# Performance work log

Hardware: AMD Instinct MI355X
Metric: run time of the kernel (lower is better)

## Reference

```python
import jax, jax.numpy as jnp
import numpy as np

N, M, D = 256, 1024, 512


def setup_inputs() -> dict:
    key = jax.random.key(0)
    ks = jax.random.split(key, 12)
    s = 1.0 / np.sqrt(D)
    return {
        "q": jax.random.normal(ks[0], (N, D), jnp.float32),
        "k": jax.random.normal(ks[1], (M, D), jnp.float32),
        "v": jax.random.normal(ks[2], (M, D), jnp.float32),
        "mask": jax.random.randint(ks[3], (N, M), 0, 2, jnp.int32),
        "WQ": jax.random.normal(ks[4], (D, D), jnp.float32) * s,
        "bQ": jax.random.normal(ks[5], (D,), jnp.float32) * s,
        "WK": jax.random.normal(ks[6], (D, D), jnp.float32) * s,
        "bK": jax.random.normal(ks[7], (D,), jnp.float32) * s,
        "WV": jax.random.normal(ks[8], (D, D), jnp.float32) * s,
        "bV": jax.random.normal(ks[9], (D,), jnp.float32) * s,
        "Ww": jax.random.normal(ks[10], (1, D), jnp.float32) * s,
        "bw": jax.random.normal(ks[11], (1,), jnp.float32) * s,
    }


def reference(q, k, v, mask, WQ, bQ, WK, bK, WV, bV, Ww, bw):
    # Linear projections (torch Linear: x @ W.T + b)
    qp = q @ WQ.T + bQ            # [N, D]
    kp = k @ WK.T + bK            # [M, D]
    vp = v @ WV.T + bV            # [M, D]
    # Additive (Bahdanau) scores: tanh(q_n + k_m) . w  -> [N, M]
    t = jnp.tanh(qp[:, None, :] + kp[None, :, :])   # [N, M, D]
    score = jnp.einsum("nmd,d->nm", t, Ww[0]) + bw[0]
    score = jnp.where(mask == 1, score, jnp.float32(-1e6))
    w = jax.nn.softmax(score, axis=1)               # softmax over keys (dim 1)
    context = jnp.einsum("nm,md->nd", w, vp)        # weighted sum over keys
    return context
```

## Files before the change

kernel.cpp:

```cpp
#include <hip/hip_runtime.h>

#define NQ 256
#define MK 1024
#define DD 512
#define CSC 2.8853900817779268f
#define L2E 1.4426950408889634f

typedef __attribute__((ext_vector_type(8))) short short8;
typedef __attribute__((ext_vector_type(4))) float floatx4;

__device__ inline int swz(int i, int d)
{
    return (((i >> 4) * 16 + (d >> 5)) << 9) | (((d >> 3) & 3) << 7)
         | ((i & 15) << 3) | (d & 7);
}

__device__ inline void bsplit(float x, unsigned short& h, unsigned short& l)
{
    unsigned u = __float_as_uint(x);
    unsigned hr = (u + 0x7FFFu + ((u >> 16) & 1u)) >> 16;
    h = (unsigned short)hr;
    float hf = __uint_as_float(hr << 16);
    unsigned ul = __float_as_uint(x - hf);
    l = (unsigned short)((ul + 0x7FFFu + ((ul >> 16) & 1u)) >> 16);
}

__global__ __launch_bounds__(256) void convert_split(
    const float* __restrict__ q, const float* __restrict__ k, const float* __restrict__ v,
    const float* __restrict__ WQ, const float* __restrict__ WK, const float* __restrict__ WV,
    unsigned short* __restrict__ qhi, unsigned short* __restrict__ qlo,
    unsigned short* __restrict__ khi, unsigned short* __restrict__ klo,
    unsigned short* __restrict__ vhi, unsigned short* __restrict__ vlo,
    unsigned short* __restrict__ wqhi, unsigned short* __restrict__ wqlo,
    unsigned short* __restrict__ wkhi, unsigned short* __restrict__ wklo,
    unsigned short* __restrict__ wvhi, unsigned short* __restrict__ wvlo)
{
    const int i4 = blockIdx.x * 256 + threadIdx.x;
    const float* src; unsigned short *dh, *dl; int li;
    if (i4 < 32768)       { src = q;  dh = qhi;  dl = qlo;  li = i4; }
    else if (i4 < 163840) { src = k;  dh = khi;  dl = klo;  li = i4 - 32768; }
    else if (i4 < 294912) { src = v;  dh = vhi;  dl = vlo;  li = i4 - 163840; }
    else if (i4 < 360448) { src = WQ; dh = wqhi; dl = wqlo; li = i4 - 294912; }
    else if (i4 < 425984) { src = WK; dh = wkhi; dl = wklo; li = i4 - 360448; }
    else                  { src = WV; dh = wvhi; dl = wvlo; li = i4 - 425984; }

    float4 x = *(const float4*)&src[li * 4];
    ushort4 h, l;
    bsplit(x.x, h.x, l.x); bsplit(x.y, h.y, l.y);
    bsplit(x.z, h.z, l.z); bsplit(x.w, h.w, l.w);

    const int e = li * 4;
    const int o = swz(e >> 9, e & 511);
    *(ushort4*)&dh[o] = h;
    *(ushort4*)&dl[o] = l;
}

__global__ __launch_bounds__(256) void proj_mfma(
    const unsigned short* __restrict__ qhi, const unsigned short* __restrict__ qlo,
    const unsigned short* __restrict__ khi, const unsigned short* __restrict__ klo,
    const unsigned short* __restrict__ vhi, const unsigned short* __restrict__ vlo,
    const unsigned short* __restrict__ wqhi, const unsigned short* __restrict__ wqlo,
    const unsigned short* __restrict__ wkhi, const unsigned short* __restrict__ wklo,
    const unsigned short* __restrict__ wvhi, const unsigned short* __restrict__ wvlo,
    const float* __restrict__ bQ, const float* __restrict__ bK, const float* __restrict__ bV,
    float* __restrict__ qs, float* __restrict__ kts, float* __restrict__ vp)
{
    int t = blockIdx.x;
    const unsigned short *Xh, *Xl, *Wh, *Wl; const float* b; int mode;
    if (t < 32)       { mode = 0; Xh = qhi; Xl = qlo; Wh = wqhi; Wl = wqlo; b = bQ; }
    else if (t < 160) { mode = 1; t -= 32;  Xh = khi; Xl = klo; Wh = wkhi; Wl = wklo; b = bK; }
    else              { mode = 2; t -= 160; Xh = vhi; Xl = vlo; Wh = wvhi; Wl = wvlo; b = bV; }
    const int i0 = (t >> 3) * 64;
    const int j0 = (t & 7) * 64;

    const int l  = threadIdx.x & 63;
    const int w  = threadIdx.x >> 6;
    const int lr = l & 15;
    const int rbase = (l >> 4) * 4;

    const unsigned short* Ah = Xh + ((i0 >> 4) + w) * 8192 + l * 8;
    const unsigned short* Al = Xl + ((i0 >> 4) + w) * 8192 + l * 8;
    const unsigned short* Bh = Wh + (j0 >> 4) * 8192 + l * 8;
    const unsigned short* Bl = Wl + (j0 >> 4) * 8192 + l * 8;

    floatx4 acc[4] = {{0,0,0,0},{0,0,0,0},{0,0,0,0},{0,0,0,0}};

#pragma unroll
    for (int kc = 0; kc < 16; ++kc) {
        short8 ah = *(const short8*)(Ah + kc * 512);
        short8 al = *(const short8*)(Al + kc * 512);
#pragma unroll
        for (int nt = 0; nt < 4; ++nt) {
            short8 bh = *(const short8*)(Bh + nt * 8192 + kc * 512);
            short8 bl = *(const short8*)(Bl + nt * 8192 + kc * 512);
            acc[nt] = __builtin_amdgcn_mfma_f32_16x16x32_bf16(ah, bh, acc[nt], 0, 0, 0);
            acc[nt] = __builtin_amdgcn_mfma_f32_16x16x32_bf16(ah, bl, acc[nt], 0, 0, 0);
            acc[nt] = __builtin_amdgcn_mfma_f32_16x16x32_bf16(al, bh, acc[nt], 0, 0, 0);
        }
    }

    if (mode == 1) {
#pragma unroll
        for (int nt = 0; nt < 4; ++nt) {
            const int d = j0 + nt * 16 + lr;
            const float bb = b[d];
            float* base = &kts[(((d >> 3) * MK) + i0 + w * 16 + rbase) * 8 + (d & 7)];
#pragma unroll
            for (int j = 0; j < 4; ++j)
                base[j * 8] = (acc[nt][j] + bb) * CSC;
        }
    } else {
        float* dst = (mode == 0) ? qs : vp;
        const float sc = (mode == 0) ? CSC : 1.0f;
#pragma unroll
        for (int nt = 0; nt < 4; ++nt) {
            const float bb = b[j0 + nt * 16 + lr];
#pragma unroll
            for (int j = 0; j < 4; ++j)
                dst[(i0 + w * 16 + rbase + j) * DD + j0 + nt * 16 + lr]
                    = (acc[nt][j] + bb) * sc;
        }
    }
}

__global__ __launch_bounds__(1024) void score_sm(
    const float* __restrict__ qs, const float* __restrict__ kts,
    const float* __restrict__ Ww, const int* __restrict__ mask,
    float* __restrict__ S)
{
    const int n = blockIdx.x;
    const int t = threadIdx.x;
    const int lane = t & 63, wave = t >> 6;

    __shared__ float qw[DD * 2];
    __shared__ float red[16];

    if (t < DD) { qw[t * 2] = qs[n * DD + t]; qw[t * 2 + 1] = Ww[t]; }
    __syncthreads();

    const float* kp = kts + t * 8;
    float acc = 0.f;
    for (int c = 0; c < 64; ++c) {
        float4 k0 = *(const float4*)(kp + c * (MK * 8));
        float4 k1 = *(const float4*)(kp + c * (MK * 8) + 4);
        float kv[8] = {k0.x, k0.y, k0.z, k0.w, k1.x, k1.y, k1.z, k1.w};
#pragma unroll
        for (int j = 0; j < 8; ++j) {
            float2 wq = *(const float2*)&qw[(c * 8 + j) * 2];
            float e = __builtin_amdgcn_exp2f(wq.x + kv[j]);
            acc = fmaf(wq.y, __builtin_amdgcn_rcpf(e + 1.0f), acc);
        }
    }

    float s = -2.0f * acc;
    s = (mask[n * MK + t] == 1) ? s : -1e6f;

    float mx = s;
    for (int o = 32; o > 0; o >>= 1) mx = fmaxf(mx, __shfl_xor(mx, o, 64));
    if (lane == 0) red[wave] = mx;
    __syncthreads();
    if (wave == 0) {
        float r = red[lane & 15];
        for (int o = 8; o > 0; o >>= 1) r = fmaxf(r, __shfl_xor(r, o, 64));
        if (lane == 0) red[0] = r;
    }
    __syncthreads();
    mx = red[0];
    __syncthreads();

    float e = __builtin_amdgcn_exp2f((s - mx) * L2E);
    float sum = e;
    for (int o = 32; o > 0; o >>= 1) sum += __shfl_xor(sum, o, 64);
    if (lane == 0) red[wave] = sum;
    __syncthreads();
    if (wave == 0) {
        float r = red[lane & 15];
        for (int o = 8; o > 0; o >>= 1) r += __shfl_xor(r, o, 64);
        if (lane == 0) red[0] = r;
    }
    __syncthreads();
    sum = red[0];

    S[n * MK + t] = e * __builtin_amdgcn_rcpf(sum);
}

#define CNG 8
#define CMC 256

__global__ __launch_bounds__(512) void context_v2(const float* __restrict__ S,
                                                  const float* __restrict__ vp,
                                                  float* __restrict__ out)
{
    __shared__ float ws[CMC][12];
    const int t = threadIdx.x;
    const int n0 = blockIdx.x * CNG;
    const int m0 = blockIdx.y * CMC;

#pragma unroll
    for (int p = 0; p < 4; ++p) {
        int e = t + p * 512;
        int m = e & 255, n = e >> 8;
        ws[m][n] = S[(n0 + n) * MK + m0 + m];
    }
    __syncthreads();

    float acc[CNG] = {};
    for (int m = 0; m < CMC; ++m) {
        float vv = vp[(m0 + m) * DD + t];
        float4 w0 = *(const float4*)&ws[m][0];
        float4 w4 = *(const float4*)&ws[m][4];
        acc[0] = fmaf(w0.x, vv, acc[0]);
        acc[1] = fmaf(w0.y, vv, acc[1]);
        acc[2] = fmaf(w0.z, vv, acc[2]);
        acc[3] = fmaf(w0.w, vv, acc[3]);
        acc[4] = fmaf(w4.x, vv, acc[4]);
        acc[5] = fmaf(w4.y, vv, acc[5]);
        acc[6] = fmaf(w4.z, vv, acc[6]);
        acc[7] = fmaf(w4.w, vv, acc[7]);
    }
#pragma unroll
    for (int n = 0; n < CNG; ++n) atomicAdd(&out[(n0 + n) * DD + t], acc[n]);
}

extern "C" void kernel_launch(void* const* d_in, const int* in_sizes, int n_in,
                              void* d_out, int out_size, void* d_ws, size_t ws_size,
                              hipStream_t stream)
{
    const float* q    = (const float*)d_in[0];
    const float* k    = (const float*)d_in[1];
    const float* v    = (const float*)d_in[2];
    const int*   mask = (const int*)  d_in[3];
    const float* WQ   = (const float*)d_in[4];
    const float* bQ   = (const float*)d_in[5];
    const float* WK   = (const float*)d_in[6];
    const float* bK   = (const float*)d_in[7];
    const float* WV   = (const float*)d_in[8];
    const float* bV   = (const float*)d_in[9];
    const float* Ww   = (const float*)d_in[10];
    const float* bw   = (const float*)d_in[11];
    (void)bw;
    float* out = (float*)d_out;

    float* qs  = (float*)d_ws;
    float* kts = qs + NQ * DD;
    float* vp  = kts + DD * MK;
    float* S   = vp + MK * DD;
    unsigned short* p16  = (unsigned short*)(S + NQ * MK);
    unsigned short* qhi  = p16;              p16 += NQ * DD;
    unsigned short* qlo  = p16;              p16 += NQ * DD;
    unsigned short* khi  = p16;              p16 += MK * DD;
    unsigned short* klo  = p16;              p16 += MK * DD;
    unsigned short* vhi  = p16;              p16 += MK * DD;
    unsigned short* vlo  = p16;              p16 += MK * DD;
    unsigned short* wqhi = p16;              p16 += DD * DD;
    unsigned short* wqlo = p16;              p16 += DD * DD;
    unsigned short* wkhi = p16;              p16 += DD * DD;
    unsigned short* wklo = p16;              p16 += DD * DD;
    unsigned short* wvhi = p16;              p16 += DD * DD;
    unsigned short* wvlo = p16;

    hipMemsetAsync(d_out, 0, (size_t)NQ * DD * sizeof(float), stream);

    convert_split<<<1920, 256, 0, stream>>>(q, k, v, WQ, WK, WV,
        qhi, qlo, khi, klo, vhi, vlo, wqhi, wqlo, wkhi, wklo, wvhi, wvlo);

    proj_mfma<<<288, 256, 0, stream>>>(qhi, qlo, khi, klo, vhi, vlo,
        wqhi, wqlo, wkhi, wklo, wvhi, wvlo, bQ, bK, bV, qs, kts, vp);

    score_sm<<<NQ, 1024, 0, stream>>>(qs, kts, Ww, mask, S);

    context_v2<<<dim3(NQ / CNG, MK / CMC), dim3(512), 0, stream>>>(S, vp, out);
}
```

Measured before the change: 158.4 us.

## Precompute exponentials of projections to remove exp from score loop; drop context atomics

Projection epilogue now stores exp2 of the scaled q and k projections, so the score inner loop computes tanh via a product instead of an exp per element. The k loads in the score loop are software-prefetched one chunk ahead. The context kernel is restructured to reduce over all keys within a block via shared memory, removing the atomics and the output memset. Factoring exp(a+b) into a product risks overflow/precision loss for large projection magnitudes.

After: 144.7 us. -8.7%, faster.

```diff
diff --git a/kernel.cpp b/kernel.cpp
--- a/kernel.cpp
+++ b/kernel.cpp
@@ -63,7 +63,7 @@
     const unsigned short* __restrict__ wkhi, const unsigned short* __restrict__ wklo,
     const unsigned short* __restrict__ wvhi, const unsigned short* __restrict__ wvlo,
     const float* __restrict__ bQ, const float* __restrict__ bK, const float* __restrict__ bV,
-    float* __restrict__ qs, float* __restrict__ kts, float* __restrict__ vp)
+    float* __restrict__ qe, float* __restrict__ ke, float* __restrict__ vp)
 {
     int t = blockIdx.x;
     const unsigned short *Xh, *Xl, *Wh, *Wl; const float* b; int mode;
@@ -104,27 +104,28 @@
         for (int nt = 0; nt < 4; ++nt) {
             const int d = j0 + nt * 16 + lr;
             const float bb = b[d];
-            float* base = &kts[(((d >> 3) * MK) + i0 + w * 16 + rbase) * 8 + (d & 7)];
+            float* base = &ke[(((d >> 3) * MK) + i0 + w * 16 + rbase) * 8 + (d & 7)];
 #pragma unroll
             for (int j = 0; j < 4; ++j)
-                base[j * 8] = (acc[nt][j] + bb) * CSC;
+                base[j * 8] = __builtin_amdgcn_exp2f((acc[nt][j] + bb) * CSC);
         }
     } else {
-        float* dst = (mode == 0) ? qs : vp;
-        const float sc = (mode == 0) ? CSC : 1.0f;
+        float* dst = (mode == 0) ? qe : vp;
 #pragma unroll
         for (int nt = 0; nt < 4; ++nt) {
             const float bb = b[j0 + nt * 16 + lr];
 #pragma unroll
-            for (int j = 0; j < 4; ++j)
-                dst[(i0 + w * 16 + rbase + j) * DD + j0 + nt * 16 + lr]
-                    = (acc[nt][j] + bb) * sc;
+            for (int j = 0; j < 4; ++j) {
+                float val = acc[nt][j] + bb;
+                if (mode == 0) val = __builtin_amdgcn_exp2f(val * CSC);
+                dst[(i0 + w * 16 + rbase + j) * DD + j0 + nt * 16 + lr] = val;
+            }
         }
     }
 }
 
 __global__ __launch_bounds__(1024) void score_sm(
-    const float* __restrict__ qs, const float* __restrict__ kts,
+    const float* __restrict__ qe, const float* __restrict__ kts,
     const float* __restrict__ Ww, const int* __restrict__ mask,
     float* __restrict__ S)
 {
@@ -135,21 +136,29 @@
     __shared__ float qw[DD * 2];
     __shared__ float red[16];
 
-    if (t < DD) { qw[t * 2] = qs[n * DD + t]; qw[t * 2 + 1] = Ww[t]; }
+    if (t < DD) { qw[t * 2] = qe[n * DD + t]; qw[t * 2 + 1] = Ww[t]; }
     __syncthreads();
 
     const float* kp = kts + t * 8;
     float acc = 0.f;
+    float4 k0 = *(const float4*)(kp);
+    float4 k1 = *(const float4*)(kp + 4);
     for (int c = 0; c < 64; ++c) {
-        float4 k0 = *(const float4*)(kp + c * (MK * 8));
-        float4 k1 = *(const float4*)(kp + c * (MK * 8) + 4);
+        float4 p0 = k0, p1 = k1;
+        if (c + 1 < 64) {
+            p0 = *(const float4*)(kp + (c + 1) * (MK * 8));
+            p1 = *(const float4*)(kp + (c + 1) * (MK * 8) + 4);
+        }
         float kv[8] = {k0.x, k0.y, k0.z, k0.w, k1.x, k1.y, k1.z, k1.w};
 #pragma unroll
-        for (int j = 0; j < 8; ++j) {
-            float2 wq = *(const float2*)&qw[(c * 8 + j) * 2];
-            float e = __builtin_amdgcn_exp2f(wq.x + kv[j]);
-            acc = fmaf(wq.y, __builtin_amdgcn_rcpf(e + 1.0f), acc);
-        }
+        for (int j = 0; j < 8; j += 2) {
+            float4 qq = *(const float4*)&qw[(c * 8 + j) * 2];
+            float e0 = qq.x * kv[j];
+            float e1 = qq.z * kv[j + 1];
+            acc = fmaf(qq.y, __builtin_amdgcn_rcpf(e0 + 1.0f), acc);
+            acc = fmaf(qq.w, __builtin_amdgcn_rcpf(e1 + 1.0f), acc);
+        }
+        k0 = p0; k1 = p1;
     }
 
     float s = -2.0f * acc;
@@ -184,42 +193,47 @@
     S[n * MK + t] = e * __builtin_amdgcn_rcpf(sum);
 }
 
-#define CNG 8
-#define CMC 256
-
-__global__ __launch_bounds__(512) void context_v2(const float* __restrict__ S,
+#define XNG 4
+
+__global__ __launch_bounds__(512) void context_v3(const float* __restrict__ S,
                                                   const float* __restrict__ vp,
                                                   float* __restrict__ out)
 {
-    __shared__ float ws[CMC][12];
+    __shared__ float ws[MK][XNG];
+    __shared__ float pacc[4][XNG][128];
     const int t = threadIdx.x;
-    const int n0 = blockIdx.x * CNG;
-    const int m0 = blockIdx.y * CMC;
-
-#pragma unroll
-    for (int p = 0; p < 4; ++p) {
+    const int n0 = blockIdx.x * XNG;
+    const int d0 = blockIdx.y * 128;
+
+#pragma unroll
+    for (int p = 0; p < 8; ++p) {
         int e = t + p * 512;
-        int m = e & 255, n = e >> 8;
-        ws[m][n] = S[(n0 + n) * MK + m0 + m];
-    }
-    __syncthreads();
-
-    float acc[CNG] = {};
-    for (int m = 0; m < CMC; ++m) {
-        float vv = vp[(m0 + m) * DD + t];
-        float4 w0 = *(const float4*)&ws[m][0];
-        float4 w4 = *(const float4*)&ws[m][4];
-        acc[0] = fmaf(w0.x, vv, acc[0]);
-        acc[1] = fmaf(w0.y, vv, acc[1]);
-        acc[2] = fmaf(w0.z, vv, acc[2]);
-        acc[3] = fmaf(w0.w, vv, acc[3]);
-        acc[4] = fmaf(w4.x, vv, acc[4]);
-        acc[5] = fmaf(w4.y, vv, acc[5]);
-        acc[6] = fmaf(w4.z, vv, acc[6]);
-        acc[7] = fmaf(w4.w, vv, acc[7]);
-    }
-#pragma unroll
-    for (int n = 0; n < CNG; ++n) atomicAdd(&out[(n0 + n) * DD + t], acc[n]);
+        int nn = e >> 10, m = e & 1023;
+        ws[m][nn] = S[(n0 + nn) * MK + m];
+    }
+    __syncthreads();
+
+    const int d = d0 + (t & 127);
+    const int seg = t >> 7;
+    float acc[XNG] = {};
+    for (int m = seg * 256; m < seg * 256 + 256; ++m) {
+        float vv = vp[m * DD + d];
+        float4 w = *(const float4*)&ws[m][0];
+        acc[0] = fmaf(w.x, vv, acc[0]);
+        acc[1] = fmaf(w.y, vv, acc[1]);
+        acc[2] = fmaf(w.z, vv, acc[2]);
+        acc[3] = fmaf(w.w, vv, acc[3]);
+    }
+#pragma unroll
+    for (int nn = 0; nn < XNG; ++nn) pacc[seg][nn][t & 127] = acc[nn];
+    __syncthreads();
+
+    if (t < XNG * 128) {
+        int nn = t >> 7, dd = t & 127;
+        float r = pacc[0][nn][dd] + pacc[1][nn][dd]
+                + pacc[2][nn][dd] + pacc[3][nn][dd];
+        out[(n0 + nn) * DD + d0 + dd] = r;
+    }
 }
 
 extern "C" void kernel_launch(void* const* d_in, const int* in_sizes, int n_in,
@@ -241,9 +255,9 @@
     (void)bw;
     float* out = (float*)d_out;
 
-    float* qs  = (float*)d_ws;
-    float* kts = qs + NQ * DD;
-    float* vp  = kts + DD * MK;
+    float* qe  = (float*)d_ws;
+    float* ke  = qe + NQ * DD;
+    float* vp  = ke + DD * MK;
     float* S   = vp + MK * DD;
     unsigned short* p16  = (unsigned short*)(S + NQ * MK);
     unsigned short* qhi  = p16;              p16 += NQ * DD;
@@ -259,15 +273,13 @@
     unsigned short* wvhi = p16;              p16 += DD * DD;
     unsigned short* wvlo = p16;
 
-    hipMemsetAsync(d_out, 0, (size_t)NQ * DD * sizeof(float), stream);
-
     convert_split<<<1920, 256, 0, stream>>>(q, k, v, WQ, WK, WV,
         qhi, qlo, khi, klo, vhi, vlo, wqhi, wqlo, wkhi, wklo, wvhi, wvlo);
 
     proj_mfma<<<288, 256, 0, stream>>>(qhi, qlo, khi, klo, vhi, vlo,
-        wqhi, wqlo, wkhi, wklo, wvhi, wvlo, bQ, bK, bV, qs, kts, vp);
-
-    score_sm<<<NQ, 1024, 0, stream>>>(qs, kts, Ww, mask, S);
-
-    context_v2<<<dim3(NQ / CNG, MK / CMC), dim3(512), 0, stream>>>(S, vp, out);
-}
+        wqhi, wqlo, wkhi, wklo, wvhi, wvlo, bQ, bK, bV, qe, ke, vp);
+
+    score_sm<<<NQ, 1024, 0, stream>>>(qe, ke, Ww, mask, S);
+
+    context_v3<<<dim3(NQ / XNG, 4), 512, 0, stream>>>(S, vp, out);
+}
```
